# Performance work log

Hardware: AMD Instinct MI355X
Metric: run time of the kernel (lower is better)

## Reference

```python
import jax, jax.numpy as jnp
import numpy as np
import math

WP, WF = 10, 10      # past/future window
EPS = 1e-8           # torch cosine_similarity eps
CLIP = 1.0 - 1e-6    # keep arccos (and its grad) finite
MAXN = 110           # hard-coded alpha width in the module


def setup_inputs() -> dict:
    key = jax.random.key(0)
    k1, k2, k3, k4, k5, k6 = jax.random.split(key, 6)
    B, L, G, N, D = 32, 110, 512, 40, 300
    node_features = jax.random.normal(k1, (B, L, G), jnp.float32)
    knowledge = jax.random.normal(k2, (B, L, N, D), jnp.float32)
    anew = jax.random.uniform(k3, (B, L, N), jnp.float32)
    var_sem = 2.0 / (G + G)
    var_con = 2.0 / (D + D)
    weight_sem = jax.random.normal(k4, (G, G), jnp.float32) * var_sem
    weight_con = jax.random.normal(k5, (D, D), jnp.float32) * var_con
    text_len = jax.random.randint(k6, (B,), 55, L + 1, jnp.int32)
    return dict(node_features=node_features, knowledge=knowledge, anew=anew,
                weight_sem=weight_sem, weight_con=weight_con, text_len=text_len)


def reference(node_features, knowledge, anew, weight_sem, weight_con, text_len):
    B, L, G = node_features.shape
    N = knowledge.shape[2]
    dt = node_features.dtype

    # window + validity mask, replaces per-(i,j) python slicing: [B, j, k]
    j = jnp.arange(L)[:, None]
    k = jnp.arange(L)[None, :]
    cur = text_len[:, None, None]
    mask = (k >= j - WP) & (k <= j + WF)
    mask = mask[None] & (k[None, :, :] <= cur - 1) & (j[None, :, :] < cur)
    fmask = mask.astype(dt)

    # ---- semantic branch: score = 1 - acos(cos_sim(f_j, W_sem f_k))/pi, windowed softmax
    att_sem = jnp.einsum('st,blt->bls', weight_sem, node_features)      # [B,L,G]
    num = jnp.einsum('bjg,bkg->bjk', node_features, att_sem)
    nf = jnp.maximum(jnp.linalg.norm(node_features, axis=-1), EPS)      # [B,L]
    na = jnp.maximum(jnp.linalg.norm(att_sem, axis=-1), EPS)            # [B,L]
    cos = num / (nf[:, :, None] * na[:, None, :])
    score = 1.0 - jnp.arccos(jnp.clip(cos, -CLIP, CLIP)) / math.pi
    neg = jnp.finfo(dt).min
    s = jnp.where(mask, score, neg)
    s = s - jnp.max(s, axis=-1, keepdims=True)
    e = jnp.exp(s) * fmask
    alphas_sem = e / jnp.maximum(jnp.sum(e, axis=-1, keepdims=True), EPS)  # [B,L,L]

    # ---- affinity transform of anew: v -> (||[v, v/2] - [0.5, 0]|| - 0.06467)/0.607468
    anew_aff = (jnp.sqrt((anew - 0.5) ** 2 + (0.5 * anew) ** 2) - 0.06467) / 0.607468

    # ---- contextual branch: windowed sum_n |cos_sim(aff_feat_{k,n}, knowledge_{j,n})|
    att_con = jnp.einsum('blns,st->blnt', knowledge, weight_con)        # [B,L,N,D]
    aff_feat = att_con * anew_aff[..., None]                            # [B,L,N,D]
    num_c = jnp.einsum('bknd,bjnd->bjkn', aff_feat, knowledge)          # [B,j,k,N]
    n_f = jnp.maximum(jnp.linalg.norm(aff_feat, axis=-1), EPS)          # [B,k,N]
    n_k = jnp.maximum(jnp.linalg.norm(knowledge, axis=-1), EPS)         # [B,j,N]
    cos_c = num_c / (n_f[:, None, :, :] * n_k[:, :, None, :])
    alphas_con = 10.0 * jnp.sum(jnp.abs(cos_c), axis=-1) * fmask        # [B,j,k]

    out = 0.5 * alphas_sem + 0.5 * alphas_con                           # [B,L,L]
    if L < MAXN:  # module hard-codes width 110
        out = jnp.pad(out, ((0, 0), (0, 0), (0, MAXN - L)))
    return out
```

## Files before the change

### kernel.cpp

```cpp
#include <hip/hip_runtime.h>
#include <hip/hip_bf16.h>
#include <math.h>

constexpr int Bb   = 32;
constexpr int Ls   = 110;
constexpr int Gs   = 512;
constexpr int Ns   = 40;
constexpr int Ds   = 300;
constexpr int WPc  = 10;
constexpr int WFc  = 10;
constexpr int MAXNc = 110;
constexpr float EPSf  = 1e-8f;
constexpr float CLIPf = 1.0f - 1e-6f;
constexpr int BL = Bb * Ls;
constexpr int Mrows = BL * Ns;
constexpr int BPITCH = 328;

typedef __attribute__((ext_vector_type(8))) short short8_t;
typedef __attribute__((ext_vector_type(4))) short short4_t;
typedef __attribute__((ext_vector_type(4))) float floatx4;

__device__ __forceinline__ unsigned short bf16r(float f) {
  unsigned u = __float_as_uint(f);
  u += 0x7fffu + ((u >> 16) & 1u);
  return (unsigned short)(u >> 16);
}

__device__ __forceinline__ unsigned pkbf(float lo, float hi) {
  unsigned a = __float_as_uint(lo), b = __float_as_uint(hi);
  a += 0x7fffu + ((a >> 16) & 1u);
  b += 0x7fffu + ((b >> 16) & 1u);
  return (a >> 16) | (b & 0xffff0000u);
}

__device__ __forceinline__ short8_t cvt8(const float4 v0, const float4 v1) {
  union { short8_t s; unsigned u[4]; } p;
  p.u[0] = pkbf(v0.x, v0.y);
  p.u[1] = pkbf(v0.z, v0.w);
  p.u[2] = pkbf(v1.x, v1.y);
  p.u[3] = pkbf(v1.z, v1.w);
  return p.s;
}

__global__ __launch_bounds__(256) void transpose_wsem(const float* __restrict__ w,
                                                      float* __restrict__ wt) {
  __shared__ float tile[32][33];
  const int bx = blockIdx.x * 32;
  const int by = blockIdx.y * 32;
  const int tx = threadIdx.x;
  const int ty = threadIdx.y;
#pragma unroll
  for (int r = ty; r < 32; r += 8)
    tile[r][tx] = w[(by + r) * Gs + (bx + tx)];
  __syncthreads();
#pragma unroll
  for (int r = ty; r < 32; r += 8)
    wt[(bx + r) * Gs + (by + tx)] = tile[tx][r];
}

__global__ __launch_bounds__(256) void wct_prep(const float* __restrict__ wc,
                                                short* __restrict__ wct) {
  __shared__ float tile[32][33];
  const int t0 = blockIdx.x * 32;
  const int s0 = blockIdx.y * 32;
  const int tx = threadIdx.x, ty = threadIdx.y;
#pragma unroll
  for (int r = ty; r < 32; r += 8) {
    const int s = s0 + r, t = t0 + tx;
    tile[r][tx] = (s < Ds && t < Ds) ? wc[s * Ds + t] : 0.f;
  }
  __syncthreads();
#pragma unroll
  for (int r = ty; r < 32; r += 8) {
    const int t = t0 + r, s = s0 + tx;
    wct[t * 320 + s] = (short)bf16r(tile[tx][r]);
  }
}

__global__ __launch_bounds__(512) void sem_gemm(const float* __restrict__ nf,
                                                const float* __restrict__ wt,
                                                float* __restrict__ att_sem,
                                                float* __restrict__ na_arr) {
  const int bl0 = blockIdx.x * 8;
  const int s = threadIdx.x;
  const float* __restrict__ x0 = nf + (size_t)bl0 * Gs;
  float acc[8];
#pragma unroll
  for (int r = 0; r < 8; ++r) acc[r] = 0.f;
#pragma unroll 4
  for (int t = 0; t < Gs; ++t) {
    const float wv = wt[t * Gs + s];
#pragma unroll
    for (int r = 0; r < 8; ++r) acc[r] = fmaf(wv, x0[r * Gs + t], acc[r]);
  }
#pragma unroll
  for (int r = 0; r < 8; ++r) att_sem[(size_t)(bl0 + r) * Gs + s] = acc[r];

  __shared__ float partial[8][8];
  const int wave = s >> 6, lane = s & 63;
#pragma unroll
  for (int r = 0; r < 8; ++r) {
    float v = acc[r] * acc[r];
#pragma unroll
    for (int off = 32; off > 0; off >>= 1) v += __shfl_xor(v, off);
    if (lane == 0) partial[r][wave] = v;
  }
  __syncthreads();
  if (s < 8) {
    float sum = 0.f;
#pragma unroll
    for (int w2 = 0; w2 < 8; ++w2) sum += partial[s][w2];
    na_arr[bl0 + s] = fmaxf(sqrtf(sum), EPSf);
  }
}

__global__ __launch_bounds__(256) void sem_attn(const float* __restrict__ nf,
                                                const float* __restrict__ att_sem,
                                                const float* __restrict__ na_arr,
                                                const int* __restrict__ tlen,
                                                float* __restrict__ out) {
  const int blk = blockIdx.x;
  const int b = blk / Ls, j = blk % Ls;
  const int len = tlen[b];
  float* __restrict__ orow = out + (size_t)(b * Ls + j) * MAXNc;
  if (j >= len) {
    for (int k = threadIdx.x; k < MAXNc; k += 256) orow[k] = 0.f;
    return;
  }
  const int k0 = max(j - WPc, 0);
  const int k1 = min(j + WFc, len - 1);
  const int nk = k1 - k0 + 1;

  __shared__ float xs[Gs];
  __shared__ float sc[21];
  __shared__ float red[4];

  const float* __restrict__ x = nf + (size_t)(b * Ls + j) * Gs;
  float ss = 0.f;
  for (int t = threadIdx.x; t < Gs; t += 256) {
    const float v = x[t];
    xs[t] = v;
    ss += v * v;
  }
  const int wave = threadIdx.x >> 6, lane = threadIdx.x & 63;
#pragma unroll
  for (int off = 32; off > 0; off >>= 1) ss += __shfl_xor(ss, off);
  if (lane == 0) red[wave] = ss;
  __syncthreads();
  const float nfn = fmaxf(sqrtf(red[0] + red[1] + red[2] + red[3]), EPSf);

  for (int i = wave; i < nk; i += 4) {
    const int k = k0 + i;
    const float* __restrict__ as = att_sem + (size_t)(b * Ls + k) * Gs;
    float d = 0.f;
#pragma unroll
    for (int t = lane; t < Gs; t += 64) d = fmaf(xs[t], as[t], d);
#pragma unroll
    for (int off = 32; off > 0; off >>= 1) d += __shfl_xor(d, off);
    if (lane == 0) {
      float cs = d / (nfn * na_arr[b * Ls + k]);
      cs = fminf(fmaxf(cs, -CLIPf), CLIPf);
      sc[i] = 1.0f - acosf(cs) * (float)(1.0 / M_PI);
    }
  }
  __syncthreads();
  if (threadIdx.x == 0) {
    float m = -1e30f;
    for (int i = 0; i < nk; ++i) m = fmaxf(m, sc[i]);
    red[0] = m;
  }
  __syncthreads();
  const float m = red[0];
  if ((int)threadIdx.x < nk) sc[threadIdx.x] = expf(sc[threadIdx.x] - m);
  __syncthreads();
  if (threadIdx.x == 0) {
    float s = 0.f;
    for (int i = 0; i < nk; ++i) s += sc[i];
    red[1] = 1.0f / fmaxf(s, EPSf);
  }
  __syncthreads();
  const float inv = red[1];
  for (int k = threadIdx.x; k < MAXNc; k += 256) {
    float v = 0.f;
    if (k >= k0 && k <= k1) v = 0.5f * sc[k - k0] * inv;
    orow[k] = v;
  }
}

__global__ __launch_bounds__(256) void con_gemm_mfma(const float* __restrict__ kn,
                                                     const short* __restrict__ wct,
                                                     const int* __restrict__ tlen,
                                                     unsigned short* __restrict__ ybar,
                                                     float* __restrict__ rowss) {
  const int row0 = blockIdx.x * 64;
  {
    const int bl0 = row0 / Ns, bl1 = (row0 + 63) / Ns;
    bool alive = false;
    for (int bl = bl0; bl <= bl1; ++bl)
      if ((bl % Ls) < tlen[bl / Ls]) alive = true;
    if (!alive) return;
  }
  const int n0 = blockIdx.y * 80;

  __shared__ short Bl[80 * BPITCH];

  const int tid = threadIdx.x;
  const int wave = tid >> 6, lane = tid & 63;
  const int quad = lane >> 4, l16 = lane & 15;

  for (int s = tid; s < 80 * 40; s += 256) {
    const int nl = s / 40, slot = s % 40;
    *reinterpret_cast<short8_t*>(&Bl[nl * BPITCH + slot * 8]) =
        *reinterpret_cast<const short8_t*>(wct + (n0 + nl) * 320 + slot * 8);
  }

  const float* __restrict__ arow = kn + (size_t)(row0 + wave * 16 + l16) * Ds;

  floatx4 acc[5];
#pragma unroll
  for (int i = 0; i < 5; ++i) acc[i] = (floatx4){0.f, 0.f, 0.f, 0.f};

  float4 A0[3], A1[3];
#pragma unroll
  for (int p = 0; p < 2; ++p) {
    const int d0 = p * 32 + quad * 8;
    A0[p] = *reinterpret_cast<const float4*>(arow + d0);
    A1[p] = *reinterpret_cast<const float4*>(arow + d0 + 4);
  }
  __syncthreads();

#pragma unroll
  for (int c = 0; c < 10; ++c) {
    if (c < 8) {
      const int pc = c + 2;
      const int d0 = pc * 32 + quad * 8;
      if (pc < 9) {
        A0[pc % 3] = *reinterpret_cast<const float4*>(arow + d0);
        A1[pc % 3] = *reinterpret_cast<const float4*>(arow + d0 + 4);
      } else {
        float4 v0 = make_float4(0.f, 0.f, 0.f, 0.f);
        float4 v1 = make_float4(0.f, 0.f, 0.f, 0.f);
        if (quad == 0) {
          v0 = *reinterpret_cast<const float4*>(arow + d0);
          v1 = *reinterpret_cast<const float4*>(arow + d0 + 4);
        } else if (quad == 1) {
          v0 = *reinterpret_cast<const float4*>(arow + d0);
        }
        A0[pc % 3] = v0;
        A1[pc % 3] = v1;
      }
    }
    const short8_t afrag = cvt8(A0[c % 3], A1[c % 3]);
#pragma unroll
    for (int i = 0; i < 5; ++i) {
      const short8_t bfrag = *reinterpret_cast<const short8_t*>(
          &Bl[(i * 16 + l16) * BPITCH + c * 32 + quad * 8]);
      acc[i] = __builtin_amdgcn_mfma_f32_16x16x32_bf16(afrag, bfrag, acc[i], 0, 0, 0);
    }
  }

#pragma unroll
  for (int r = 0; r < 4; ++r) {
    float p = 0.f;
#pragma unroll
    for (int i = 0; i < 5; ++i) {
      const float y = acc[i][r];
      p = fmaf(y, y, p);
    }
    p += __shfl_xor(p, 1);
    p += __shfl_xor(p, 2);
    p += __shfl_xor(p, 4);
    p += __shfl_xor(p, 8);
    if (l16 == 0)
      atomicAdd(&rowss[row0 + wave * 16 + quad * 4 + r], p);
  }

#pragma unroll
  for (int i = 0; i < 5; ++i) {
    const int col = n0 + i * 16 + l16;
    if (col < Ds) {
#pragma unroll
      for (int r = 0; r < 4; ++r) {
        const int row = row0 + wave * 16 + quad * 4 + r;
        ybar[(size_t)row * Ds + col] = bf16r(acc[i][r]);
      }
    }
  }
}

__global__ __launch_bounds__(512) void con_attn_mfma(const float* __restrict__ kn,
                                                     const unsigned short* __restrict__ ybar,
                                                     const float* __restrict__ rowss,
                                                     const float* __restrict__ anew,
                                                     const int* __restrict__ tlen,
                                                     float* __restrict__ out) {
  const int b = blockIdx.x / 7;
  const int jt = blockIdx.x % 7;
  const int j0 = jt * 16;
  const int len = tlen[b];
  if (j0 >= len) return;
  const int kbase = min(max(j0 - WPc, 0), Ls - 48);

  const int tid = threadIdx.x;
  const int wave = tid >> 6, lane = tid & 63;
  const int quad = lane >> 4, l16 = lane & 15;

  __shared__ float red[8][768];

  const int jj = min(j0 + l16, Ls - 1);
  const size_t blj = (size_t)(b * Ls + jj);

  float outacc[3][4];
#pragma unroll
  for (int t = 0; t < 3; ++t)
#pragma unroll
    for (int r = 0; r < 4; ++r) outacc[t][r] = 0.f;

  const unsigned short* yrow[3];
  int krow_m[3];
#pragma unroll
  for (int t = 0; t < 3; ++t) {
    const int k = kbase + t * 16 + l16;
    yrow[t] = ybar + ((size_t)(b * Ls + k) * Ns) * Ds;
    krow_m[t] = (b * Ls + k) * Ns;
  }

  for (int ni = 0; ni < 5; ++ni) {
    const int n = wave + ni * 8;
    const float* __restrict__ arow = kn + (blj * Ns + n) * Ds;

    float w_t[3];
#pragma unroll
    for (int t = 0; t < 3; ++t) {
      const int m = krow_m[t] + n;
      const float a = anew[m];
      const float ssqk = rowss[m];
      const float aff = (sqrtf((a - 0.5f) * (a - 0.5f) + 0.25f * a * a) - 0.06467f) *
                        (1.0f / 0.607468f);
      w_t[t] = aff / fmaxf(aff * sqrtf(ssqk), EPSf);
    }

    floatx4 S[3];
#pragma unroll
    for (int t = 0; t < 3; ++t) S[t] = (floatx4){0.f, 0.f, 0.f, 0.f};
    float ssq = 0.f;

#pragma unroll
    for (int c = 0; c < 10; ++c) {
      const int d0 = c * 32 + quad * 8;
      float av[8];
      if (c < 9) {
        const float4 v0 = *reinterpret_cast<const float4*>(arow + d0);
        const float4 v1 = *reinterpret_cast<const float4*>(arow + d0 + 4);
        av[0] = v0.x; av[1] = v0.y; av[2] = v0.z; av[3] = v0.w;
        av[4] = v1.x; av[5] = v1.y; av[6] = v1.z; av[7] = v1.w;
      } else {
        if (quad == 0) {
          const float4 v0 = *reinterpret_cast<const float4*>(arow + d0);
          const float4 v1 = *reinterpret_cast<const float4*>(arow + d0 + 4);
          av[0] = v0.x; av[1] = v0.y; av[2] = v0.z; av[3] = v0.w;
          av[4] = v1.x; av[5] = v1.y; av[6] = v1.z; av[7] = v1.w;
        } else if (quad == 1) {
          const float4 v0 = *reinterpret_cast<const float4*>(arow + d0);
          av[0] = v0.x; av[1] = v0.y; av[2] = v0.z; av[3] = v0.w;
          av[4] = av[5] = av[6] = av[7] = 0.f;
        } else {
#pragma unroll
          for (int e = 0; e < 8; ++e) av[e] = 0.f;
        }
      }
      short8_t afrag;
#pragma unroll
      for (int e = 0; e < 8; ++e) {
        ssq = fmaf(av[e], av[e], ssq);
        afrag[e] = (short)bf16r(av[e]);
      }
#pragma unroll
      for (int t = 0; t < 3; ++t) {
        const unsigned short* yr = yrow[t] + (size_t)n * Ds;
        short8_t bfrag;
        if (c < 9) {
          const short4_t u0 = *reinterpret_cast<const short4_t*>(yr + d0);
          const short4_t u1 = *reinterpret_cast<const short4_t*>(yr + d0 + 4);
          bfrag[0] = u0.x; bfrag[1] = u0.y; bfrag[2] = u0.z; bfrag[3] = u0.w;
          bfrag[4] = u1.x; bfrag[5] = u1.y; bfrag[6] = u1.z; bfrag[7] = u1.w;
        } else {
          if (quad == 0) {
            const short4_t u0 = *reinterpret_cast<const short4_t*>(yr + d0);
            const short4_t u1 = *reinterpret_cast<const short4_t*>(yr + d0 + 4);
            bfrag[0] = u0.x; bfrag[1] = u0.y; bfrag[2] = u0.z; bfrag[3] = u0.w;
            bfrag[4] = u1.x; bfrag[5] = u1.y; bfrag[6] = u1.z; bfrag[7] = u1.w;
          } else if (quad == 1) {
            const short4_t u0 = *reinterpret_cast<const short4_t*>(yr + d0);
            bfrag[0] = u0.x; bfrag[1] = u0.y; bfrag[2] = u0.z; bfrag[3] = u0.w;
            bfrag[4] = bfrag[5] = bfrag[6] = bfrag[7] = 0;
          } else {
#pragma unroll
            for (int e = 0; e < 8; ++e) bfrag[e] = 0;
          }
        }
        S[t] = __builtin_amdgcn_mfma_f32_16x16x32_bf16(afrag, bfrag, S[t], 0, 0, 0);
      }
    }

    ssq += __shfl_xor(ssq, 16);
    ssq += __shfl_xor(ssq, 32);
    const float kinv = 1.0f / fmaxf(sqrtf(ssq), EPSf);

#pragma unroll
    for (int r = 0; r < 4; ++r) {
      const float kv = __shfl(kinv, quad * 4 + r);
#pragma unroll
      for (int t = 0; t < 3; ++t)
        outacc[t][r] = fmaf(kv * w_t[t], fabsf(S[t][r]), outacc[t][r]);
    }
  }

#pragma unroll
  for (int t = 0; t < 3; ++t)
#pragma unroll
    for (int r = 0; r < 4; ++r)
      red[wave][(quad * 4 + r) * 48 + t * 16 + l16] = outacc[t][r];
  __syncthreads();

  for (int idx = tid; idx < 768; idx += 512) {
    float s = 0.f;
#pragma unroll
    for (int w = 0; w < 8; ++w) s += red[w][idx];
    const int j = j0 + idx / 48;
    const int k = kbase + idx % 48;
    if (j < len && k < len && k >= j - WPc && k <= j + WFc)
      out[(size_t)(b * Ls + j) * MAXNc + k] += 5.0f * s;
  }
}

extern "C" void kernel_launch(void* const* d_in, const int* in_sizes, int n_in,
                              void* d_out, int out_size, void* d_ws, size_t ws_size,
                              hipStream_t stream) {
  const float* nf   = (const float*)d_in[0];
  const float* kn   = (const float*)d_in[1];
  const float* anew = (const float*)d_in[2];
  const float* wsem = (const float*)d_in[3];
  const float* wcon = (const float*)d_in[4];
  const int*   tlen = (const int*)d_in[5];
  float* out = (float*)d_out;

  float* att_sem = (float*)d_ws;
  float* na_arr  = att_sem + (size_t)BL * Gs;
  float* wt      = na_arr + BL;
  short* wct     = (short*)(wt + (size_t)Gs * Gs);
  float* rowss   = (float*)(wct + 320 * 320);
  unsigned short* ybar = (unsigned short*)(rowss + Mrows);

  hipMemsetAsync(rowss, 0, (size_t)Mrows * sizeof(float), stream);
  transpose_wsem<<<dim3(16, 16), dim3(32, 8), 0, stream>>>(wsem, wt);
  wct_prep<<<dim3(10, 10), dim3(32, 8), 0, stream>>>(wcon, wct);
  sem_gemm<<<BL / 8, 512, 0, stream>>>(nf, wt, att_sem, na_arr);
  sem_attn<<<BL, 256, 0, stream>>>(nf, att_sem, na_arr, tlen, out);
  con_gemm_mfma<<<dim3(Mrows / 64, 4), 256, 0, stream>>>(kn, wct, tlen, ybar, rowss);
  con_attn_mfma<<<Bb * 7, 512, 0, stream>>>(kn, ybar, rowss, anew, tlen, out);
}
```

Measured before the change: 513.2 us.

## Amortize weight tile load over 256 rows per block with XCD-aware block mapping

The contextual projection GEMM now has each block process 256 rows (four 16-row tiles per wave) instead of 64, so the 80x300 bf16 weight slice loaded into shared memory is reused four times as often. A 1D grid is remapped so blocks on the same XCD handle all four column slices of the same row group, aiming to improve L2 reuse of the knowledge rows. Dead-row skipping moves to per-16-row-tile granularity, and the A-prefetch depth grows to four chunks with a launch-bounds occupancy hint. The trade-off is fewer blocks, with serialized tiles per wave and less latency hiding between tiles.

After: 497.0 us. 1.03x faster.

```diff
diff --git a/kernel.cpp b/kernel.cpp
--- a/kernel.cpp
+++ b/kernel.cpp
@@ -15,6 +15,7 @@
 constexpr int BL = Bb * Ls;
 constexpr int Mrows = BL * Ns;
 constexpr int BPITCH = 328;
+constexpr int RGRP = Mrows / 256;
 
 typedef __attribute__((ext_vector_type(8))) short short8_t;
 typedef __attribute__((ext_vector_type(4))) short short4_t;
@@ -187,57 +188,62 @@
   }
 }
 
-__global__ __launch_bounds__(256) void con_gemm_mfma(const float* __restrict__ kn,
-                                                     const short* __restrict__ wct,
-                                                     const int* __restrict__ tlen,
-                                                     unsigned short* __restrict__ ybar,
-                                                     float* __restrict__ rowss) {
-  const int row0 = blockIdx.x * 64;
-  {
-    const int bl0 = row0 / Ns, bl1 = (row0 + 63) / Ns;
-    bool alive = false;
-    for (int bl = bl0; bl <= bl1; ++bl)
-      if ((bl % Ls) < tlen[bl / Ls]) alive = true;
-    if (!alive) return;
-  }
-  const int n0 = blockIdx.y * 80;
+__global__ __launch_bounds__(256, 3) void con_gemm_mfma(const float* __restrict__ kn,
+                                                        const short* __restrict__ wct,
+                                                        const int* __restrict__ tlen,
+                                                        unsigned short* __restrict__ ybar,
+                                                        float* __restrict__ rowss) {
+  const int lin = blockIdx.x;
+  const int xcd = lin & 7, slot = lin >> 3;
+  const int m = slot & 3;
+  const int g = xcd + 8 * (slot >> 2);
+  if (g >= RGRP) return;
+  const int rowbase = g * 256;
+  const int n0 = m * 80;
 
   __shared__ short Bl[80 * BPITCH];
-
   const int tid = threadIdx.x;
+  for (int s = tid; s < 80 * 40; s += 256) {
+    const int nl = s / 40, sl = s % 40;
+    *reinterpret_cast<short8_t*>(&Bl[nl * BPITCH + sl * 8]) =
+        *reinterpret_cast<const short8_t*>(wct + (n0 + nl) * 320 + sl * 8);
+  }
+  __syncthreads();
+
   const int wave = tid >> 6, lane = tid & 63;
   const int quad = lane >> 4, l16 = lane & 15;
 
-  for (int s = tid; s < 80 * 40; s += 256) {
-    const int nl = s / 40, slot = s % 40;
-    *reinterpret_cast<short8_t*>(&Bl[nl * BPITCH + slot * 8]) =
-        *reinterpret_cast<const short8_t*>(wct + (n0 + nl) * 320 + slot * 8);
-  }
-
-  const float* __restrict__ arow = kn + (size_t)(row0 + wave * 16 + l16) * Ds;
-
-  floatx4 acc[5];
-#pragma unroll
-  for (int i = 0; i < 5; ++i) acc[i] = (floatx4){0.f, 0.f, 0.f, 0.f};
-
-  float4 A0[3], A1[3];
-#pragma unroll
-  for (int p = 0; p < 2; ++p) {
-    const int d0 = p * 32 + quad * 8;
-    A0[p] = *reinterpret_cast<const float4*>(arow + d0);
-    A1[p] = *reinterpret_cast<const float4*>(arow + d0 + 4);
-  }
-  __syncthreads();
-
-#pragma unroll
-  for (int c = 0; c < 10; ++c) {
-    if (c < 8) {
-      const int pc = c + 2;
-      const int d0 = pc * 32 + quad * 8;
+#pragma unroll
+  for (int tt = 0; tt < 4; ++tt) {
+    const int row0 = rowbase + wave * 64 + tt * 16;
+    const int blA = row0 / Ns, blB = (row0 + 15) / Ns;
+    const bool alive = ((blA % Ls) < tlen[blA / Ls]) | ((blB % Ls) < tlen[blB / Ls]);
+    if (!alive) continue;
+
+    const float* __restrict__ arow = kn + (size_t)(row0 + l16) * Ds;
+
+    float4 A0[4], A1[4];
+#pragma unroll
+    for (int p = 0; p < 4; ++p) {
+      const int d0 = p * 32 + quad * 8;
+      A0[p] = *reinterpret_cast<const float4*>(arow + d0);
+      A1[p] = *reinterpret_cast<const float4*>(arow + d0 + 4);
+    }
+
+    floatx4 acc[5];
+#pragma unroll
+    for (int i = 0; i < 5; ++i) acc[i] = (floatx4){0.f, 0.f, 0.f, 0.f};
+
+#pragma unroll
+    for (int c = 0; c < 10; ++c) {
+      const short8_t afrag = cvt8(A0[c & 3], A1[c & 3]);
+      const int pc = c + 4;
       if (pc < 9) {
-        A0[pc % 3] = *reinterpret_cast<const float4*>(arow + d0);
-        A1[pc % 3] = *reinterpret_cast<const float4*>(arow + d0 + 4);
-      } else {
+        const int d0 = pc * 32 + quad * 8;
+        A0[c & 3] = *reinterpret_cast<const float4*>(arow + d0);
+        A1[c & 3] = *reinterpret_cast<const float4*>(arow + d0 + 4);
+      } else if (pc == 9) {
+        const int d0 = 288 + quad * 8;
         float4 v0 = make_float4(0.f, 0.f, 0.f, 0.f);
         float4 v1 = make_float4(0.f, 0.f, 0.f, 0.f);
         if (quad == 0) {
@@ -246,43 +252,35 @@
         } else if (quad == 1) {
           v0 = *reinterpret_cast<const float4*>(arow + d0);
         }
-        A0[pc % 3] = v0;
-        A1[pc % 3] = v1;
-      }
-    }
-    const short8_t afrag = cvt8(A0[c % 3], A1[c % 3]);
+        A0[c & 3] = v0;
+        A1[c & 3] = v1;
+      }
+#pragma unroll
+      for (int i = 0; i < 5; ++i) {
+        const short8_t bfrag = *reinterpret_cast<const short8_t*>(
+            &Bl[(i * 16 + l16) * BPITCH + c * 32 + quad * 8]);
+        acc[i] = __builtin_amdgcn_mfma_f32_16x16x32_bf16(afrag, bfrag, acc[i], 0, 0, 0);
+      }
+    }
+
+#pragma unroll
+    for (int r = 0; r < 4; ++r) {
+      float p = 0.f;
+#pragma unroll
+      for (int i = 0; i < 5; ++i) p = fmaf(acc[i][r], acc[i][r], p);
+      p += __shfl_xor(p, 1);
+      p += __shfl_xor(p, 2);
+      p += __shfl_xor(p, 4);
+      p += __shfl_xor(p, 8);
+      if (l16 == 0) atomicAdd(&rowss[row0 + quad * 4 + r], p);
+    }
 #pragma unroll
     for (int i = 0; i < 5; ++i) {
-      const short8_t bfrag = *reinterpret_cast<const short8_t*>(
-          &Bl[(i * 16 + l16) * BPITCH + c * 32 + quad * 8]);
-      acc[i] = __builtin_amdgcn_mfma_f32_16x16x32_bf16(afrag, bfrag, acc[i], 0, 0, 0);
-    }
-  }
-
-#pragma unroll
-  for (int r = 0; r < 4; ++r) {
-    float p = 0.f;
-#pragma unroll
-    for (int i = 0; i < 5; ++i) {
-      const float y = acc[i][r];
-      p = fmaf(y, y, p);
-    }
-    p += __shfl_xor(p, 1);
-    p += __shfl_xor(p, 2);
-    p += __shfl_xor(p, 4);
-    p += __shfl_xor(p, 8);
-    if (l16 == 0)
-      atomicAdd(&rowss[row0 + wave * 16 + quad * 4 + r], p);
-  }
-
-#pragma unroll
-  for (int i = 0; i < 5; ++i) {
-    const int col = n0 + i * 16 + l16;
-    if (col < Ds) {
-#pragma unroll
-      for (int r = 0; r < 4; ++r) {
-        const int row = row0 + wave * 16 + quad * 4 + r;
-        ybar[(size_t)row * Ds + col] = bf16r(acc[i][r]);
+      const int col = n0 + i * 16 + l16;
+      if (col < Ds) {
+#pragma unroll
+        for (int r = 0; r < 4; ++r)
+          ybar[(size_t)(row0 + quad * 4 + r) * Ds + col] = bf16r(acc[i][r]);
       }
     }
   }
@@ -332,9 +330,9 @@
     float w_t[3];
 #pragma unroll
     for (int t = 0; t < 3; ++t) {
-      const int m = krow_m[t] + n;
-      const float a = anew[m];
-      const float ssqk = rowss[m];
+      const int mm = krow_m[t] + n;
+      const float a = anew[mm];
+      const float ssqk = rowss[mm];
       const float aff = (sqrtf((a - 0.5f) * (a - 0.5f) + 0.25f * a * a) - 0.06467f) *
                         (1.0f / 0.607468f);
       w_t[t] = aff / fmaxf(aff * sqrtf(ssqk), EPSf);
@@ -457,6 +455,6 @@
   wct_prep<<<dim3(10, 10), dim3(32, 8), 0, stream>>>(wcon, wct);
   sem_gemm<<<BL / 8, 512, 0, stream>>>(nf, wt, att_sem, na_arr);
   sem_attn<<<BL, 256, 0, stream>>>(nf, att_sem, na_arr, tlen, out);
-  con_gemm_mfma<<<dim3(Mrows / 64, 4), 256, 0, stream>>>(kn, wct, tlen, ybar, rowss);
+  con_gemm_mfma<<<2208, 256, 0, stream>>>(kn, wct, tlen, ybar, rowss);
   con_attn_mfma<<<Bb * 7, 512, 0, stream>>>(kn, ybar, rowss, anew, tlen, out);
 }
```
